# Kernel optimization log

Hardware: AMD Instinct MI355X
Metric: run time of the kernel (lower is better)

The kernel has to match this reference:

```python
import jax, jax.numpy as jnp
import numpy as np

BETA = 0.25

def setup_inputs() -> dict:
    key = jax.random.key(0)
    k1, k2 = jax.random.split(key)
    B, L, D, K = 8, 4096, 512, 8192
    z_e = jax.random.normal(k1, (B, L, D), dtype=jnp.float32)
    # codebook init: uniform(-1/K, 1/K) as in the torch module
    embeddings = jax.random.uniform(k2, (K, D), dtype=jnp.float32,
                                    minval=-1.0 / K, maxval=1.0 / K)
    return {"z_e": z_e, "embeddings": embeddings}


def reference(z_e, embeddings):
    B, L, D = z_e.shape
    z_flat = z_e.reshape(-1, D)  # [N, D], N = B*L
    # squared euclidean distances: ||z||^2 - 2 z.E^T + ||E||^2
    # (argmin identical to torch.cdist argmin; avoids sqrt)
    d2 = (jnp.sum(z_flat * z_flat, axis=1, keepdims=True)
          - 2.0 * jnp.einsum('nd,kd->nk', z_flat, embeddings)
          + jnp.sum(embeddings * embeddings, axis=1)[None, :])  # [N, K]
    encoding_indices = jnp.argmin(d2, axis=1)  # [N]
    z_q = embeddings[encoding_indices].reshape(B, L, D)
    commitment_loss = BETA * jnp.mean((jax.lax.stop_gradient(z_q) - z_e) ** 2)
    embedding_loss = jnp.mean((jax.lax.stop_gradient(z_e) - z_q) ** 2)
    vq_loss = commitment_loss + embedding_loss
    # straight-through estimator
    z_q_st = z_e + jax.lax.stop_gradient(z_q - z_e)
    return z_q_st, vq_loss, encoding_indices.reshape(B, L)
```

## Files before the change

kernel.cpp:

```cpp
#include <hip/hip_runtime.h>
#include <math.h>

#define DIM    512
#define KCB    8192
#define NROWS  32768

typedef _Float16 f16x8 __attribute__((ext_vector_type(8)));
typedef float    f32x4 __attribute__((ext_vector_type(4)));

#define OFF_ZH    0ull
#define OFF_EH    33554432ull
#define OFF_EE    41943040ull
#define OFF_ZZ    41975808ull
#define OFF_CNT   42106880ull
#define OFF_LOSS  42237952ull
#define OFF_CAND  42237960ull
#define WS_NEEDED_64  50757640ull
#define WS_NEEDED_128 59146248ull
#define THR 2.048f
#define SCORE_OFS 512.0f
#define PRUNE_MARGIN 2.6f

__device__ __forceinline__ void gl_lds16(const void* g, void* l) {
    __builtin_amdgcn_global_load_lds(
        (const __attribute__((address_space(1))) unsigned int*)g,
        (__attribute__((address_space(3))) unsigned int*)l, 16, 0, 0);
}

__global__ __launch_bounds__(256)
void cvt_all(const float* __restrict__ Z, const float* __restrict__ E,
             _Float16* __restrict__ Zh, _Float16* __restrict__ Eh) {
    const int i = blockIdx.x * 256 + threadIdx.x;
    const float* in; _Float16* out; float scale; size_t c;
    if (i < NROWS * DIM / 8) { in = Z; out = Zh; scale = 1.0f;    c = (size_t)i; }
    else { in = E; out = Eh; scale = 8192.0f; c = (size_t)(i - NROWS * DIM / 8); }
    const float4* p = (const float4*)in + c * 2;
    float4 v0 = p[0], v1 = p[1];
    f16x8 h;
    h[0] = (_Float16)(v0.x * scale); h[1] = (_Float16)(v0.y * scale);
    h[2] = (_Float16)(v0.z * scale); h[3] = (_Float16)(v0.w * scale);
    h[4] = (_Float16)(v1.x * scale); h[5] = (_Float16)(v1.y * scale);
    h[6] = (_Float16)(v1.z * scale); h[7] = (_Float16)(v1.w * scale);
    *(f16x8*)(out + c * 8) = h;
}

__device__ __forceinline__ float blk128_sq(const float* __restrict__ p) {
    const float4* a4 = (const float4*)p;
    float4 v0 = a4[0], v1 = a4[1];
    float r[8];
    r[0] = __fmul_rn(v0.x, v0.x); r[1] = __fmul_rn(v0.y, v0.y);
    r[2] = __fmul_rn(v0.z, v0.z); r[3] = __fmul_rn(v0.w, v0.w);
    r[4] = __fmul_rn(v1.x, v1.x); r[5] = __fmul_rn(v1.y, v1.y);
    r[6] = __fmul_rn(v1.z, v1.z); r[7] = __fmul_rn(v1.w, v1.w);
#pragma unroll
    for (int i = 1; i < 16; ++i) {
        v0 = a4[i * 2]; v1 = a4[i * 2 + 1];
        r[0] = __fadd_rn(r[0], __fmul_rn(v0.x, v0.x));
        r[1] = __fadd_rn(r[1], __fmul_rn(v0.y, v0.y));
        r[2] = __fadd_rn(r[2], __fmul_rn(v0.z, v0.z));
        r[3] = __fadd_rn(r[3], __fmul_rn(v0.w, v0.w));
        r[4] = __fadd_rn(r[4], __fmul_rn(v1.x, v1.x));
        r[5] = __fadd_rn(r[5], __fmul_rn(v1.y, v1.y));
        r[6] = __fadd_rn(r[6], __fmul_rn(v1.z, v1.z));
        r[7] = __fadd_rn(r[7], __fmul_rn(v1.w, v1.w));
    }
    return __fadd_rn(__fadd_rn(__fadd_rn(r[0], r[1]), __fadd_rn(r[2], r[3])),
                     __fadd_rn(__fadd_rn(r[4], r[5]), __fadd_rn(r[6], r[7])));
}

__global__ __launch_bounds__(256)
void norms_kernel(const float* __restrict__ Z, const float* __restrict__ E,
                  float* __restrict__ zz, float* __restrict__ ee,
                  unsigned int* __restrict__ cnt, unsigned int* __restrict__ rowmax,
                  double* __restrict__ lossAcc) {
    const int id = blockIdx.x * 256 + threadIdx.x;
    const int row = id >> 2, b = id & 3;
    if (id == 0) *lossAcc = 0.0;
    const float* p = (row < NROWS ? Z + (size_t)row * DIM
                                  : E + (size_t)(row - NROWS) * DIM) + b * 128;
    float blk = blk128_sq(p);
    float v1 = __fadd_rn(blk, __shfl_xor(blk, 1, 64));
    float v2 = __fadd_rn(v1, __shfl_xor(v1, 2, 64));
    if (b == 0) {
        if (row < NROWS) { zz[row] = v2; cnt[row] = 0; rowmax[row] = 0u; }
        else             ee[row - NROWS] = v2;
    }
}

__global__ __launch_bounds__(256, 4)
void screen_kernel(const _Float16* __restrict__ Zh, const _Float16* __restrict__ Eh,
                   unsigned int* __restrict__ cnt, unsigned int* __restrict__ cand,
                   unsigned int* __restrict__ rowmax, const int cap) {
    __shared__ __align__(16) char lds[16384];

    const int tid = threadIdx.x;
    const int l = tid & 63;
    const int w = tid >> 6;
    const int wrow = w >> 1;
    const int wcol = w & 1;
    const int rowBase = (int)(blockIdx.x & 255) * 128;
    const int colBase = (int)(blockIdx.x >> 8) * 128;

#define STAGE(ks) do {                                                         \
        _Pragma("unroll")                                                      \
        for (int _i = 0; _i < 2; ++_i) {                                       \
            const int _u = tid + _i * 256;                                     \
            const int _r = _u >> 2;                                            \
            const int _s = (_u & 3) ^ ((_r >> 1) & 3);                         \
            gl_lds16(Zh + (size_t)(rowBase + _r) * DIM + (ks) * 32 + _s * 8,   \
                     lds + (w * 64 + _i * 256) * 16 + l * 16);                 \
            gl_lds16(Eh + (size_t)(colBase + _r) * DIM + (ks) * 32 + _s * 8,   \
                     lds + 8192 + (w * 64 + _i * 256) * 16 + l * 16);          \
        }                                                                      \
    } while (0)

    int offA[4], offB[4];
#pragma unroll
    for (int m = 0; m < 4; ++m) {
        const int rr = wrow * 64 + m * 16 + (l & 15);
        offA[m] = (rr * 4 + ((l >> 4) ^ ((rr >> 1) & 3))) * 16;
    }
#pragma unroll
    for (int n = 0; n < 4; ++n) {
        const int c = wcol * 64 + n * 16 + (l & 15);
        offB[n] = 8192 + (c * 4 + ((l >> 4) ^ ((c >> 1) & 3))) * 16;
    }

    f32x4 acc[4][4];
#pragma unroll
    for (int m = 0; m < 4; ++m)
#pragma unroll
        for (int n = 0; n < 4; ++n) acc[m][n] = (f32x4){0.f, 0.f, 0.f, 0.f};

    for (int ks = 0; ks < 16; ++ks) {
        STAGE(ks);
        __syncthreads();
        f16x8 af[4], bf[4];
#pragma unroll
        for (int m = 0; m < 4; ++m) af[m] = *(const f16x8*)(lds + offA[m]);
#pragma unroll
        for (int n = 0; n < 4; ++n) bf[n] = *(const f16x8*)(lds + offB[n]);
#pragma unroll
        for (int m = 0; m < 4; ++m)
#pragma unroll
            for (int n = 0; n < 4; ++n)
                acc[m][n] = __builtin_amdgcn_mfma_f32_16x16x32_f16(af[m], bf[n], acc[m][n], 0, 0, 0);
        if (ks < 15) __syncthreads();
    }

#pragma unroll
    for (int m = 0; m < 4; ++m) {
#pragma unroll
        for (int r = 0; r < 4; ++r) {
            float mx = fmaxf(fmaxf(acc[m][0][r], acc[m][1][r]),
                             fmaxf(acc[m][2][r], acc[m][3][r]));
#pragma unroll
            for (int off = 1; off < 16; off <<= 1)
                mx = fmaxf(mx, __shfl_xor(mx, off, 64));
            const int rowg = rowBase + wrow * 64 + m * 16 + (l >> 4) * 4 + r;
            const float mxs = fmaxf(mx, -256.0f) + SCORE_OFS;
            unsigned old = 0;
            if ((l & 15) == 0)
                old = atomicMax(&rowmax[rowg], __float_as_uint(mxs));
            old = __shfl(old, l & 48, 64);
            const float cur = fmaxf(__uint_as_float(old), mxs);
            const float thr = cur - SCORE_OFS - THR;
#pragma unroll
            for (int n = 0; n < 4; ++n) {
                if (acc[m][n][r] >= thr) {
                    unsigned pos = atomicAdd(&cnt[rowg], 1u);
                    if (pos < (unsigned)cap) {
                        unsigned kidx = (unsigned)(colBase + wcol * 64 + n * 16 + (l & 15));
                        float sc = fmaxf(acc[m][n][r] + SCORE_OFS, 1.0f);
                        cand[(size_t)rowg * cap + pos] =
                            (__float_as_uint(sc) & 0xFFFFE000u) | kidx;
                    }
                }
            }
        }
    }
#undef STAGE
}

__global__ __launch_bounds__(256)
void finish_kernel(const float* __restrict__ Z, const float* __restrict__ E,
                   const float* __restrict__ zz, const float* __restrict__ ee,
                   const unsigned int* __restrict__ cnt,
                   const unsigned int* __restrict__ cand,
                   float* __restrict__ outZ, float* __restrict__ outIdxF,
                   double* __restrict__ lossAcc, const int cap) {
    __shared__ double psum[4];
    const int tid = threadIdx.x;
    const int l = tid & 63;
    const int w = tid >> 6;
    double s = 0.0;

    for (int j = 0; j < 8; ++j) {
        const int row = blockIdx.x * 32 + w * 8 + j;
        const unsigned c = cnt[row];
        int kk;
        if (c == 1) {
            kk = (int)(cand[(size_t)row * cap] & 0x1FFFu);
        } else if (c >= 2 && c <= (unsigned)cap) {
            const unsigned key1 = (l < (int)c) ? cand[(size_t)row * cap + l] : 0u;
            const unsigned key2 = ((int)c > 64 && l + 64 < (int)c)
                                      ? cand[(size_t)row * cap + l + 64] : 0u;
            const float s1 = __uint_as_float(key1 & 0xFFFFE000u);
            const float s2 = __uint_as_float(key2 & 0xFFFFE000u);
            float smax = fmaxf(s1, s2);
#pragma unroll
            for (int off = 1; off < 64; off <<= 1)
                smax = fmaxf(smax, __shfl_xor(smax, off, 64));
            const float cut = smax - PRUNE_MARGIN;

            float d2 = __builtin_inff();
            int kl = 0x7FFFFFFF;
            const float4* zr4 = (const float4*)(Z + (size_t)row * DIM);
            if (l < (int)c && s1 >= cut) {
                int k = (int)(key1 & 0x1FFFu);
                const float4* er4 = (const float4*)(E + (size_t)k * DIM);
                float acc = 0.0f;
#pragma unroll 8
                for (int i = 0; i < DIM / 4; ++i) {
                    float4 z4 = zr4[i], e4 = er4[i];
                    acc = __builtin_fmaf(z4.x, e4.x, acc);
                    acc = __builtin_fmaf(z4.y, e4.y, acc);
                    acc = __builtin_fmaf(z4.z, e4.z, acc);
                    acc = __builtin_fmaf(z4.w, e4.w, acc);
                }
                float t = __builtin_fmaf(-2.0f, acc, zz[row]);
                d2 = __fadd_rn(t, ee[k]);
                kl = k;
            }
            if ((int)c > 64 && l + 64 < (int)c && s2 >= cut) {
                int k = (int)(key2 & 0x1FFFu);
                const float4* er4 = (const float4*)(E + (size_t)k * DIM);
                float acc = 0.0f;
#pragma unroll 8
                for (int i = 0; i < DIM / 4; ++i) {
                    float4 z4 = zr4[i], e4 = er4[i];
                    acc = __builtin_fmaf(z4.x, e4.x, acc);
                    acc = __builtin_fmaf(z4.y, e4.y, acc);
                    acc = __builtin_fmaf(z4.z, e4.z, acc);
                    acc = __builtin_fmaf(z4.w, e4.w, acc);
                }
                float t = __builtin_fmaf(-2.0f, acc, zz[row]);
                float d = __fadd_rn(t, ee[k]);
                if (d < d2 || (d == d2 && k < kl)) { d2 = d; kl = k; }
            }
#pragma unroll
            for (int off = 32; off > 0; off >>= 1) {
                float od = __shfl_down(d2, off, 64);
                int ok = __shfl_down(kl, off, 64);
                if (od < d2 || (od == d2 && ok < kl)) { d2 = od; kl = ok; }
            }
            kk = __shfl(kl, 0, 64);
        } else {
            float d2 = __builtin_inff();
            int kl = 0x7FFFFFFF;
            const float4* zr4 = (const float4*)(Z + (size_t)row * DIM);
            for (int k = l; k < KCB; k += 64) {
                const float4* er4 = (const float4*)(E + (size_t)k * DIM);
                float acc = 0.0f;
#pragma unroll 8
                for (int i = 0; i < DIM / 4; ++i) {
                    float4 z4 = zr4[i], e4 = er4[i];
                    acc = __builtin_fmaf(z4.x, e4.x, acc);
                    acc = __builtin_fmaf(z4.y, e4.y, acc);
                    acc = __builtin_fmaf(z4.z, e4.z, acc);
                    acc = __builtin_fmaf(z4.w, e4.w, acc);
                }
                float t = __builtin_fmaf(-2.0f, acc, zz[row]);
                float d = __fadd_rn(t, ee[k]);
                if (d < d2) { d2 = d; kl = k; }
            }
#pragma unroll
            for (int off = 32; off > 0; off >>= 1) {
                float od = __shfl_down(d2, off, 64);
                int ok = __shfl_down(kl, off, 64);
                if (od < d2 || (od == d2 && ok < kl)) { d2 = od; kl = ok; }
            }
            kk = __shfl(kl, 0, 64);
        }
        const float* zr = Z + (size_t)row * DIM;
        const float* er = E + (size_t)kk * DIM;
        float* orow = outZ + (size_t)row * DIM;
#pragma unroll
        for (int i = 0; i < 2; ++i) {
            int off = (l + i * 64) * 4;
            float4 z4 = *(const float4*)(zr + off);
            float4 e4 = *(const float4*)(er + off);
            float dx = __fsub_rn(e4.x, z4.x);
            float dy = __fsub_rn(e4.y, z4.y);
            float dz = __fsub_rn(e4.z, z4.z);
            float dw = __fsub_rn(e4.w, z4.w);
            float4 st;
            st.x = __fadd_rn(z4.x, dx);
            st.y = __fadd_rn(z4.y, dy);
            st.z = __fadd_rn(z4.z, dz);
            st.w = __fadd_rn(z4.w, dw);
            *(float4*)(orow + off) = st;
            s += (double)dx * dx + (double)dy * dy + (double)dz * dz + (double)dw * dw;
        }
        if (l == 0) outIdxF[row] = (float)kk;
    }
#pragma unroll
    for (int o = 32; o > 0; o >>= 1) s += __shfl_down(s, o, 64);
    if (l == 0) psum[w] = s;
    __syncthreads();
    if (tid == 0)
        atomicAdd(lossAcc, psum[0] + psum[1] + psum[2] + psum[3]);
}

__global__ void finalize_kernel(const double* __restrict__ lossAcc,
                                float* __restrict__ outLoss) {
    double m = *lossAcc / (double)((size_t)NROWS * DIM);
    float mf = (float)m;
    float c = __fmul_rn(0.25f, mf);
    *outLoss = __fadd_rn(c, mf);
}

__device__ __forceinline__ float pairwise512_sq(const float* __restrict__ p) {
    float blk[4];
#pragma unroll
    for (int b = 0; b < 4; ++b) {
        const float* a = p + b * 128;
        float r[8];
#pragma unroll
        for (int j = 0; j < 8; ++j) r[j] = __fmul_rn(a[j], a[j]);
#pragma unroll
        for (int i = 8; i < 128; i += 8) {
#pragma unroll
            for (int j = 0; j < 8; ++j)
                r[j] = __fadd_rn(r[j], __fmul_rn(a[i + j], a[i + j]));
        }
        blk[b] = __fadd_rn(__fadd_rn(__fadd_rn(r[0], r[1]), __fadd_rn(r[2], r[3])),
                           __fadd_rn(__fadd_rn(r[4], r[5]), __fadd_rn(r[6], r[7])));
    }
    return __fadd_rn(__fadd_rn(blk[0], blk[1]), __fadd_rn(blk[2], blk[3]));
}

__global__ void ee_kernel(const float* __restrict__ E, float* __restrict__ ee) {
    int k = blockIdx.x * blockDim.x + threadIdx.x;
    if (k < KCB) ee[k] = pairwise512_sq(E + (size_t)k * DIM);
}

__global__ __launch_bounds__(512, 2)
void argmin_fallback(const float* __restrict__ Z, const float* __restrict__ E,
                     const float* __restrict__ ee, int* __restrict__ outIdx) {
    __shared__ __align__(16) char smem[(32 * 132 + 32 * 260) * 4];
    float (*As)[132] = (float (*)[132])smem;
    float (*Bs)[260] = (float (*)[260])(smem + 32 * 132 * 4);
    __shared__ float zzs[128];
    const int tid = threadIdx.x;
    const int tx = tid & 31;
    const int ty = tid >> 5;
    const int rowBase = blockIdx.x * 128;
    if (tid < 128) zzs[tid] = pairwise512_sq(Z + (size_t)(rowBase + tid) * DIM);
    __syncthreads();
    float zz[8];
#pragma unroll
    for (int m = 0; m < 8; ++m) zz[m] = zzs[ty * 8 + m];
    float bestV[8]; int bestI[8];
#pragma unroll
    for (int m = 0; m < 8; ++m) { bestV[m] = __builtin_inff(); bestI[m] = 0; }
    for (int tile = 0; tile < 32; ++tile) {
        float acc[8][8];
#pragma unroll
        for (int m = 0; m < 8; ++m)
#pragma unroll
            for (int n = 0; n < 8; ++n) acc[m][n] = 0.0f;
        for (int kc = 0; kc < DIM; kc += 32) {
            __syncthreads();
#pragma unroll
            for (int i = 0; i < 2; ++i) {
                int id4 = tid + i * 512;
                int r = id4 >> 3, c = id4 & 7;
                float4 v = *(const float4*)(Z + (size_t)(rowBase + r) * DIM + kc + c * 4);
                As[c * 4 + 0][r] = v.x; As[c * 4 + 1][r] = v.y;
                As[c * 4 + 2][r] = v.z; As[c * 4 + 3][r] = v.w;
            }
#pragma unroll
            for (int i = 0; i < 4; ++i) {
                int id4 = tid + i * 512;
                int r = id4 >> 3, c = id4 & 7;
                float4 v = *(const float4*)(E + (size_t)(tile * 256 + r) * DIM + kc + c * 4);
                Bs[c * 4 + 0][r] = v.x; Bs[c * 4 + 1][r] = v.y;
                Bs[c * 4 + 2][r] = v.z; Bs[c * 4 + 3][r] = v.w;
            }
            __syncthreads();
#pragma unroll
            for (int kk = 0; kk < 32; ++kk) {
                float a[8], b[8];
                *(float4*)&a[0] = *(const float4*)&As[kk][ty * 8];
                *(float4*)&a[4] = *(const float4*)&As[kk][ty * 8 + 4];
                *(float4*)&b[0] = *(const float4*)&Bs[kk][tx * 8];
                *(float4*)&b[4] = *(const float4*)&Bs[kk][tx * 8 + 4];
#pragma unroll
                for (int m = 0; m < 8; ++m)
#pragma unroll
                    for (int n = 0; n < 8; ++n)
                        acc[m][n] = __builtin_fmaf(a[m], b[n], acc[m][n]);
            }
        }
#pragma unroll
        for (int m = 0; m < 8; ++m) {
#pragma unroll
            for (int n = 0; n < 8; ++n) {
                float t = __builtin_fmaf(-2.0f, acc[m][n], zz[m]);
                float d2 = __fadd_rn(t, ee[tile * 256 + tx * 8 + n]);
                int kidx = tile * 256 + tx * 8 + n;
                if (d2 < bestV[m]) { bestV[m] = d2; bestI[m] = kidx; }
            }
        }
    }
    __syncthreads();
    float (*redV)[33] = (float (*)[33])smem;
    int   (*redI)[33] = (int (*)[33])(smem + 128 * 33 * 4);
#pragma unroll
    for (int m = 0; m < 8; ++m) {
        redV[ty * 8 + m][tx] = bestV[m];
        redI[ty * 8 + m][tx] = bestI[m];
    }
    __syncthreads();
    if (tid < 128) {
        float bv = redV[tid][0]; int bi = redI[tid][0];
        for (int j = 1; j < 32; ++j) {
            float v = redV[tid][j]; int ii = redI[tid][j];
            if (v < bv || (v == bv && ii < bi)) { bv = v; bi = ii; }
        }
        outIdx[rowBase + tid] = bi;
    }
}

__global__ void gather_kernel(const float* __restrict__ Z, const float* __restrict__ E,
                              const int* __restrict__ idx, float* __restrict__ outZ,
                              float* __restrict__ outIdxF, double* __restrict__ lossAcc) {
    int row = blockIdx.x;
    int t = threadIdx.x;
    int k = idx[row];
    const float* zr = Z + (size_t)row * DIM;
    const float* er = E + (size_t)k * DIM;
    float* orow = outZ + (size_t)row * DIM;
    double s = 0.0;
#pragma unroll
    for (int i = 0; i < 2; ++i) {
        int off = (t + i * 64) * 4;
        float4 z4 = *(const float4*)(zr + off);
        float4 e4 = *(const float4*)(er + off);
        float dx = __fsub_rn(e4.x, z4.x);
        float dy = __fsub_rn(e4.y, z4.y);
        float dz = __fsub_rn(e4.z, z4.z);
        float dw = __fsub_rn(e4.w, z4.w);
        float4 st;
        st.x = __fadd_rn(z4.x, dx);
        st.y = __fadd_rn(z4.y, dy);
        st.z = __fadd_rn(z4.z, dz);
        st.w = __fadd_rn(z4.w, dw);
        *(float4*)(orow + off) = st;
        s += (double)dx * dx + (double)dy * dy + (double)dz * dz + (double)dw * dw;
    }
#pragma unroll
    for (int o = 32; o > 0; o >>= 1) s += __shfl_down(s, o, 64);
    if (t == 0) {
        atomicAdd(lossAcc, s);
        outIdxF[row] = (float)k;
    }
}

extern "C" void kernel_launch(void* const* d_in, const int* in_sizes, int n_in,
                              void* d_out, int out_size, void* d_ws, size_t ws_size,
                              hipStream_t stream) {
    const float* Z = (const float*)d_in[0];
    const float* E = (const float*)d_in[1];
    float* out = (float*)d_out;
    float* zq_out = out;
    float* loss_out = out + (size_t)NROWS * DIM;
    float* idxf_out = loss_out + 1;

    if (ws_size >= WS_NEEDED_64) {
        const int cap = (ws_size >= WS_NEEDED_128) ? 128 : 64;
        _Float16* Zh = (_Float16*)((char*)d_ws + OFF_ZH);
        _Float16* Eh = (_Float16*)((char*)d_ws + OFF_EH);
        float* ee = (float*)((char*)d_ws + OFF_EE);
        float* zz = (float*)((char*)d_ws + OFF_ZZ);
        unsigned int* cnt = (unsigned int*)((char*)d_ws + OFF_CNT);
        unsigned int* cand = (unsigned int*)((char*)d_ws + OFF_CAND);
        unsigned int* rowmax = (unsigned int*)((char*)d_ws + OFF_CAND
                                               + (size_t)NROWS * cap * 4);
        double* lossAcc = (double*)((char*)d_ws + OFF_LOSS);

        cvt_all<<<(NROWS + KCB) * (DIM / 8) / 256, 256, 0, stream>>>(Z, E, Zh, Eh);
        norms_kernel<<<(NROWS + KCB) * 4 / 256, 256, 0, stream>>>(Z, E, zz, ee,
                                                                  cnt, rowmax, lossAcc);
        screen_kernel<<<256 * 64, 256, 0, stream>>>(Zh, Eh, cnt, cand, rowmax, cap);
        finish_kernel<<<NROWS / 32, 256, 0, stream>>>(Z, E, zz, ee, cnt, cand,
                                                      zq_out, idxf_out, lossAcc, cap);
        finalize_kernel<<<1, 1, 0, stream>>>(lossAcc, loss_out);
    } else {
        float* ee = (float*)d_ws;
        int* idx = (int*)((char*)d_ws + 32768);
        double* lossAcc = (double*)((char*)d_ws + 163840);
        hipMemsetAsync(lossAcc, 0, sizeof(double), stream);
        ee_kernel<<<KCB / 256, 256, 0, stream>>>(E, ee);
        argmin_fallback<<<NROWS / 128, 512, 0, stream>>>(Z, E, ee, idx);
        gather_kernel<<<NROWS, 64, 0, stream>>>(Z, E, idx, zq_out, idxf_out, lossAcc);
        finalize_kernel<<<1, 1, 0, stream>>>(lossAcc, loss_out);
    }
}
```

Before: 750.7 us.

## Fuse fp16 conversion into norms kernel and double K-step per barrier in screen GEMM

Merges the fp16 conversion kernel into the norms kernel, so Z and E are read from global memory once rather than twice and one launch is removed. The screen GEMM now stages two 32-wide K slices per synchronization into a 32 KB LDS buffer, halving barrier count and giving larger batches of in-flight loads. The launch-bounds occupancy hint rises from 4 to 5. The fused prep kernel has less parallelism per thread with strided per-thread stores, and the doubled LDS may limit occupancy.

```diff
diff --git a/kernel.cpp b/kernel.cpp
--- a/kernel.cpp
+++ b/kernel.cpp
@@ -27,24 +27,8 @@
         (__attribute__((address_space(3))) unsigned int*)l, 16, 0, 0);
 }
 
-__global__ __launch_bounds__(256)
-void cvt_all(const float* __restrict__ Z, const float* __restrict__ E,
-             _Float16* __restrict__ Zh, _Float16* __restrict__ Eh) {
-    const int i = blockIdx.x * 256 + threadIdx.x;
-    const float* in; _Float16* out; float scale; size_t c;
-    if (i < NROWS * DIM / 8) { in = Z; out = Zh; scale = 1.0f;    c = (size_t)i; }
-    else { in = E; out = Eh; scale = 8192.0f; c = (size_t)(i - NROWS * DIM / 8); }
-    const float4* p = (const float4*)in + c * 2;
-    float4 v0 = p[0], v1 = p[1];
-    f16x8 h;
-    h[0] = (_Float16)(v0.x * scale); h[1] = (_Float16)(v0.y * scale);
-    h[2] = (_Float16)(v0.z * scale); h[3] = (_Float16)(v0.w * scale);
-    h[4] = (_Float16)(v1.x * scale); h[5] = (_Float16)(v1.y * scale);
-    h[6] = (_Float16)(v1.z * scale); h[7] = (_Float16)(v1.w * scale);
-    *(f16x8*)(out + c * 8) = h;
-}
-
-__device__ __forceinline__ float blk128_sq(const float* __restrict__ p) {
+__device__ __forceinline__ float blk128_sq_cvt(const float* __restrict__ p,
+                                               _Float16* __restrict__ o, float scale) {
     const float4* a4 = (const float4*)p;
     float4 v0 = a4[0], v1 = a4[1];
     float r[8];
@@ -52,6 +36,14 @@
     r[2] = __fmul_rn(v0.z, v0.z); r[3] = __fmul_rn(v0.w, v0.w);
     r[4] = __fmul_rn(v1.x, v1.x); r[5] = __fmul_rn(v1.y, v1.y);
     r[6] = __fmul_rn(v1.z, v1.z); r[7] = __fmul_rn(v1.w, v1.w);
+    {
+        f16x8 h;
+        h[0] = (_Float16)(v0.x * scale); h[1] = (_Float16)(v0.y * scale);
+        h[2] = (_Float16)(v0.z * scale); h[3] = (_Float16)(v0.w * scale);
+        h[4] = (_Float16)(v1.x * scale); h[5] = (_Float16)(v1.y * scale);
+        h[6] = (_Float16)(v1.z * scale); h[7] = (_Float16)(v1.w * scale);
+        *(f16x8*)o = h;
+    }
 #pragma unroll
     for (int i = 1; i < 16; ++i) {
         v0 = a4[i * 2]; v1 = a4[i * 2 + 1];
@@ -63,22 +55,35 @@
         r[5] = __fadd_rn(r[5], __fmul_rn(v1.y, v1.y));
         r[6] = __fadd_rn(r[6], __fmul_rn(v1.z, v1.z));
         r[7] = __fadd_rn(r[7], __fmul_rn(v1.w, v1.w));
+        f16x8 h;
+        h[0] = (_Float16)(v0.x * scale); h[1] = (_Float16)(v0.y * scale);
+        h[2] = (_Float16)(v0.z * scale); h[3] = (_Float16)(v0.w * scale);
+        h[4] = (_Float16)(v1.x * scale); h[5] = (_Float16)(v1.y * scale);
+        h[6] = (_Float16)(v1.z * scale); h[7] = (_Float16)(v1.w * scale);
+        *(f16x8*)(o + i * 8) = h;
     }
     return __fadd_rn(__fadd_rn(__fadd_rn(r[0], r[1]), __fadd_rn(r[2], r[3])),
                      __fadd_rn(__fadd_rn(r[4], r[5]), __fadd_rn(r[6], r[7])));
 }
 
 __global__ __launch_bounds__(256)
-void norms_kernel(const float* __restrict__ Z, const float* __restrict__ E,
+void prep2_kernel(const float* __restrict__ Z, const float* __restrict__ E,
+                  _Float16* __restrict__ Zh, _Float16* __restrict__ Eh,
                   float* __restrict__ zz, float* __restrict__ ee,
                   unsigned int* __restrict__ cnt, unsigned int* __restrict__ rowmax,
                   double* __restrict__ lossAcc) {
     const int id = blockIdx.x * 256 + threadIdx.x;
     const int row = id >> 2, b = id & 3;
     if (id == 0) *lossAcc = 0.0;
-    const float* p = (row < NROWS ? Z + (size_t)row * DIM
-                                  : E + (size_t)(row - NROWS) * DIM) + b * 128;
-    float blk = blk128_sq(p);
+    float blk;
+    if (row < NROWS) {
+        blk = blk128_sq_cvt(Z + (size_t)row * DIM + b * 128,
+                            Zh + (size_t)row * DIM + b * 128, 1.0f);
+    } else {
+        const int k = row - NROWS;
+        blk = blk128_sq_cvt(E + (size_t)k * DIM + b * 128,
+                            Eh + (size_t)k * DIM + b * 128, 8192.0f);
+    }
     float v1 = __fadd_rn(blk, __shfl_xor(blk, 1, 64));
     float v2 = __fadd_rn(v1, __shfl_xor(v1, 2, 64));
     if (b == 0) {
@@ -87,11 +92,11 @@
     }
 }
 
-__global__ __launch_bounds__(256, 4)
+__global__ __launch_bounds__(256, 5)
 void screen_kernel(const _Float16* __restrict__ Zh, const _Float16* __restrict__ Eh,
                    unsigned int* __restrict__ cnt, unsigned int* __restrict__ cand,
                    unsigned int* __restrict__ rowmax, const int cap) {
-    __shared__ __align__(16) char lds[16384];
+    __shared__ __align__(16) char lds[32768];
 
     const int tid = threadIdx.x;
     const int l = tid & 63;
@@ -101,16 +106,16 @@
     const int rowBase = (int)(blockIdx.x & 255) * 128;
     const int colBase = (int)(blockIdx.x >> 8) * 128;
 
-#define STAGE(ks) do {                                                         \
+#define STAGEH(ks, base) do {                                                  \
         _Pragma("unroll")                                                      \
         for (int _i = 0; _i < 2; ++_i) {                                       \
             const int _u = tid + _i * 256;                                     \
             const int _r = _u >> 2;                                            \
             const int _s = (_u & 3) ^ ((_r >> 1) & 3);                         \
             gl_lds16(Zh + (size_t)(rowBase + _r) * DIM + (ks) * 32 + _s * 8,   \
-                     lds + (w * 64 + _i * 256) * 16 + l * 16);                 \
+                     lds + (base) + (w * 64 + _i * 256) * 16 + l * 16);        \
             gl_lds16(Eh + (size_t)(colBase + _r) * DIM + (ks) * 32 + _s * 8,   \
-                     lds + 8192 + (w * 64 + _i * 256) * 16 + l * 16);          \
+                     lds + (base) + 8192 + (w * 64 + _i * 256) * 16 + l * 16); \
         }                                                                      \
     } while (0)
 
@@ -132,20 +137,25 @@
 #pragma unroll
         for (int n = 0; n < 4; ++n) acc[m][n] = (f32x4){0.f, 0.f, 0.f, 0.f};
 
-    for (int ks = 0; ks < 16; ++ks) {
-        STAGE(ks);
+    for (int ph = 0; ph < 8; ++ph) {
+        STAGEH(2 * ph,     0);
+        STAGEH(2 * ph + 1, 16384);
         __syncthreads();
-        f16x8 af[4], bf[4];
-#pragma unroll
-        for (int m = 0; m < 4; ++m) af[m] = *(const f16x8*)(lds + offA[m]);
-#pragma unroll
-        for (int n = 0; n < 4; ++n) bf[n] = *(const f16x8*)(lds + offB[n]);
-#pragma unroll
-        for (int m = 0; m < 4; ++m)
-#pragma unroll
-            for (int n = 0; n < 4; ++n)
-                acc[m][n] = __builtin_amdgcn_mfma_f32_16x16x32_f16(af[m], bf[n], acc[m][n], 0, 0, 0);
-        if (ks < 15) __syncthreads();
+#pragma unroll
+        for (int h = 0; h < 2; ++h) {
+            const char* B = lds + h * 16384;
+            f16x8 af[4], bf[4];
+#pragma unroll
+            for (int m = 0; m < 4; ++m) af[m] = *(const f16x8*)(B + offA[m]);
+#pragma unroll
+            for (int n = 0; n < 4; ++n) bf[n] = *(const f16x8*)(B + offB[n]);
+#pragma unroll
+            for (int m = 0; m < 4; ++m)
+#pragma unroll
+                for (int n = 0; n < 4; ++n)
+                    acc[m][n] = __builtin_amdgcn_mfma_f32_16x16x32_f16(af[m], bf[n], acc[m][n], 0, 0, 0);
+        }
+        if (ph < 7) __syncthreads();
     }
 
 #pragma unroll
@@ -179,7 +189,7 @@
             }
         }
     }
-#undef STAGE
+#undef STAGEH
 }
 
 __global__ __launch_bounds__(256)
@@ -490,8 +500,7 @@
                                                + (size_t)NROWS * cap * 4);
         double* lossAcc = (double*)((char*)d_ws + OFF_LOSS);
 
-        cvt_all<<<(NROWS + KCB) * (DIM / 8) / 256, 256, 0, stream>>>(Z, E, Zh, Eh);
-        norms_kernel<<<(NROWS + KCB) * 4 / 256, 256, 0, stream>>>(Z, E, zz, ee,
+        prep2_kernel<<<(NROWS + KCB) * 4 / 256, 256, 0, stream>>>(Z, E, Zh, Eh, zz, ee,
                                                                   cnt, rowmax, lossAcc);
         screen_kernel<<<256 * 64, 256, 0, stream>>>(Zh, Eh, cnt, cand, rowmax, cap);
         finish_kernel<<<NROWS / 32, 256, 0, stream>>>(Z, E, zz, ee, cnt, cand,
```

New measurement: 1.025 ms. +36.5%, slower.
